# Kernel optimization log

Measured on AMD Instinct MI355X. Metric: run time of the kernel, lower is better.

## Reference

```python
import jax, jax.numpy as jnp
import numpy as np

NEG_BIG = -1e9

def setup_inputs() -> dict:
    key = jax.random.key(0)
    kq, kk, kv, kwq, kwk, kwv, km = jax.random.split(key, 7)
    B, S, d = 16, 1024, 512
    Q = jax.random.normal(kq, (B, S, d), dtype=jnp.float32)
    K = jax.random.normal(kk, (B, S, d), dtype=jnp.float32)
    V = jax.random.normal(kv, (B, S, d), dtype=jnp.float32)
    # nn.Linear weights [d, d]; torch applies x @ W.T
    WQ = jax.random.normal(kwq, (d, d), dtype=jnp.float32) / np.sqrt(d)
    WK = jax.random.normal(kwk, (d, d), dtype=jnp.float32) / np.sqrt(d)
    WV = jax.random.normal(kwv, (d, d), dtype=jnp.float32) / np.sqrt(d)
    mask = jax.random.randint(km, (B, S), 0, 2, dtype=jnp.int32)
    return {"Q": Q, "K": K, "V": V, "WQ": WQ, "WK": WK, "WV": WV, "mask": mask}


def reference(Q, K, V, WQ, WK, WV, mask):
    d = Q.shape[-1]
    q = jnp.einsum('bsd,ed->bse', Q, WQ)
    k = jnp.einsum('bsd,ed->bse', K, WK)
    v = jnp.einsum('bsd,ed->bse', V, WV)
    scores = jnp.einsum('bqd,bkd->bqk', q, k) / jnp.sqrt(jnp.float32(d))
    attn = jax.nn.softmax(scores, axis=-1)
    # Faithful to original: mask applied AFTER softmax with -1e9 fill
    m = mask[:, None, :]  # [B,1,S] broadcast over query dim
    attn = jnp.where(m == 0, jnp.float32(NEG_BIG), attn)
    out = jnp.einsum('bqk,bkd->bqd', attn, v)
    return (out, attn)
```

## Files before the change

kernel.cpp:

```cpp
#include <hip/hip_runtime.h>
#include <hip/hip_bf16.h>

typedef float f32x4 __attribute__((ext_vector_type(4)));
typedef __bf16 bf16x8 __attribute__((ext_vector_type(8)));
typedef unsigned short u16x8 __attribute__((ext_vector_type(8)));
typedef int i32x4 __attribute__((ext_vector_type(4)));

#define NEG_BIG_F (-1000000000.0f)
#define SCALE_F 0.044194173824159216f

__device__ __forceinline__ unsigned short f2bf(float f) {
  unsigned int u = __float_as_uint(f);
  u += 0x7FFFu + ((u >> 16) & 1u);
  return (unsigned short)(u >> 16);
}

__device__ __forceinline__ float bf2f(unsigned short h) {
  return __uint_as_float((unsigned int)h << 16);
}

__device__ __forceinline__ u16x8 cvt8(f32x4 a, f32x4 b) {
  u16x8 r;
  r[0] = f2bf(a[0]); r[1] = f2bf(a[1]); r[2] = f2bf(a[2]); r[3] = f2bf(a[3]);
  r[4] = f2bf(b[0]); r[5] = f2bf(b[1]); r[6] = f2bf(b[2]); r[7] = f2bf(b[3]);
  return r;
}

__device__ __forceinline__ void gload16(const void* g, char* l) {
  __builtin_amdgcn_global_load_lds(
      (const __attribute__((address_space(1))) unsigned int*)g,
      (__attribute__((address_space(3))) unsigned int*)l, 16, 0, 0);
}

__global__ __launch_bounds__(256) void cvtW(
    const float* __restrict__ w0, const float* __restrict__ w1,
    const float* __restrict__ w2, unsigned short* __restrict__ out)
{
  const float* src = blockIdx.z == 0 ? w0 : (blockIdx.z == 1 ? w1 : w2);
  unsigned short* dst = out + (size_t)blockIdx.z * 262144;
  const int i = (blockIdx.x * 256 + threadIdx.x) * 8;
  f32x4 a = *(const f32x4*)(src + i);
  f32x4 b = *(const f32x4*)(src + i + 4);
  *(u16x8*)&dst[i] = cvt8(a, b);
}

__global__ __launch_bounds__(512, 2) void proj_all(
    const float* __restrict__ Q, const float* __restrict__ Kx,
    const float* __restrict__ V, const unsigned short* __restrict__ wb,
    unsigned short* __restrict__ qb, unsigned short* __restrict__ kb,
    unsigned short* __restrict__ vt)
{
  __shared__ __align__(16) unsigned short lds[32768];

  const int bid = blockIdx.x;
  const int tid = threadIdx.x;
  const int lane = tid & 63, wave = tid >> 6;
  const int fr = lane & 15, fq = lane >> 4;

  if (bid < 256) {
    const int z = bid >> 7, rem = bid & 127;
    const float* X = z ? Kx : Q;
    const unsigned short* W = wb + (size_t)z * 262144;
    unsigned short* Y = z ? kb : qb;
    const int m0 = (rem & 63) * 256, n0 = (rem >> 6) * 256;
    const int wr = (wave >> 2) * 128, wc = (wave & 3) * 64;

    unsigned short (*As)[256][32] = (unsigned short (*)[256][32])lds;
    unsigned short (*Bs)[256][32] = (unsigned short (*)[256][32])(lds + 16384);

    f32x4 acc[8][4] = {};

    int arow_s[2], aswz_s[2];
    const float* gAs[2];
    #pragma unroll
    for (int i = 0; i < 2; i++) {
      const int c = tid + 512 * i;
      arow_s[i] = c >> 2;
      aswz_s[i] = ((c & 3) ^ ((arow_s[i] >> 1) & 3)) * 8;
      gAs[i] = X + (size_t)(m0 + arow_s[i]) * 512 + (c & 3) * 8;
    }
    const unsigned short* gB[2]; char* lB[2];
    #pragma unroll
    for (int i = 0; i < 2; i++) {
      const int c = tid + 512 * i, row = c >> 2, slot = c & 3;
      gB[i] = W + (size_t)(n0 + row) * 512 + (slot ^ ((row >> 1) & 3)) * 8;
      lB[i] = (char*)(lds + 16384) + c * 16;
    }

    f32x4 pa[2][2][2];
    #pragma unroll
    for (int i = 0; i < 2; i++) {
      pa[0][i][0] = *(const f32x4*)(gAs[i]);
      pa[0][i][1] = *(const f32x4*)(gAs[i] + 4);
      pa[1][i][0] = *(const f32x4*)(gAs[i] + 32);
      pa[1][i][1] = *(const f32x4*)(gAs[i] + 36);
    }
    #pragma unroll
    for (int i = 0; i < 2; i++) gload16(gB[i], lB[i]);
    #pragma unroll
    for (int i = 0; i < 2; i++)
      *(u16x8*)&As[0][arow_s[i]][aswz_s[i]] = cvt8(pa[0][i][0], pa[0][i][1]);

    #pragma unroll
    for (int t = 0; t < 16; t++) {
      const int cur = t & 1, nxt = cur ^ 1;
      const int kt = t * 32;
      if (t < 15) {
        #pragma unroll
        for (int i = 0; i < 2; i++) gload16(gB[i] + kt + 32, lB[i] + nxt * 16384);
      }
      if (t < 14) {
        #pragma unroll
        for (int i = 0; i < 2; i++) {
          pa[cur][i][0] = *(const f32x4*)(gAs[i] + kt + 64);
          pa[cur][i][1] = *(const f32x4*)(gAs[i] + kt + 68);
        }
      }
      if (t == 0 || t == 14)
        asm volatile("s_waitcnt vmcnt(6) lgkmcnt(0)" ::: "memory");
      else if (t == 15)
        asm volatile("s_waitcnt vmcnt(0) lgkmcnt(0)" ::: "memory");
      else
        asm volatile("s_waitcnt vmcnt(10) lgkmcnt(0)" ::: "memory");
      __builtin_amdgcn_sched_barrier(0);
      __builtin_amdgcn_s_barrier();

      bf16x8 bv[4];
      #pragma unroll
      for (int nf = 0; nf < 4; nf++) {
        const int br = wc + nf * 16 + fr;
        bv[nf] = *(const bf16x8*)&Bs[cur][br][(fq ^ ((br >> 1) & 3)) * 8];
      }
      #pragma unroll
      for (int mf = 0; mf < 8; mf++) {
        const int ar = wr + mf * 16 + fr;
        bf16x8 av = *(const bf16x8*)&As[cur][ar][(fq ^ ((ar >> 1) & 3)) * 8];
        #pragma unroll
        for (int nf = 0; nf < 4; nf++)
          acc[mf][nf] = __builtin_amdgcn_mfma_f32_16x16x32_bf16(av, bv[nf], acc[mf][nf], 0, 0, 0);
      }

      if (t < 15) {
        #pragma unroll
        for (int i = 0; i < 2; i++)
          *(u16x8*)&As[nxt][arow_s[i]][aswz_s[i]] = cvt8(pa[nxt][i][0], pa[nxt][i][1]);
      }
      __builtin_amdgcn_s_barrier();
    }

    #pragma unroll
    for (int mf = 0; mf < 8; mf++)
      #pragma unroll
      for (int nf = 0; nf < 4; nf++)
        #pragma unroll
        for (int rr = 0; rr < 4; rr++) {
          const int m = m0 + wr + mf * 16 + fq * 4 + rr;
          const int n = n0 + wc + nf * 16 + fr;
          Y[(size_t)m * 512 + n] = f2bf(acc[mf][nf][rr]);
        }
  } else {
    const int c0 = bid - 256;
    const int m0 = (c0 & 3) * 128, n0 = ((c0 >> 2) & 3) * 256, b = c0 >> 4;
    const int wr = (wave >> 2) * 64, wc = (wave & 3) * 64;
    const unsigned short* wv = wb + 524288;

    unsigned short (*As)[128][32] = (unsigned short (*)[128][32])lds;
    unsigned short (*Bs)[256][32] = (unsigned short (*)[256][32])(lds + 8192);

    f32x4 acc[4][4] = {};

    const int ar_s = tid >> 2, aslot = tid & 3;
    const unsigned short* gA = wv + (size_t)(m0 + ar_s) * 512 + (aslot ^ ((ar_s >> 1) & 3)) * 8;
    char* lA = (char*)lds + tid * 16;

    int brow_s[2], bswz_s[2];
    const float* gBs[2];
    #pragma unroll
    for (int i = 0; i < 2; i++) {
      const int c = tid + 512 * i;
      brow_s[i] = c >> 2;
      bswz_s[i] = ((c & 3) ^ ((brow_s[i] >> 1) & 3)) * 8;
      gBs[i] = V + ((size_t)b * 1024 + n0 + brow_s[i]) * 512 + (c & 3) * 8;
    }

    f32x4 pb[2][2][2];
    #pragma unroll
    for (int i = 0; i < 2; i++) {
      pb[0][i][0] = *(const f32x4*)(gBs[i]);
      pb[0][i][1] = *(const f32x4*)(gBs[i] + 4);
      pb[1][i][0] = *(const f32x4*)(gBs[i] + 32);
      pb[1][i][1] = *(const f32x4*)(gBs[i] + 36);
    }
    gload16(gA, lA);
    #pragma unroll
    for (int i = 0; i < 2; i++)
      *(u16x8*)&Bs[0][brow_s[i]][bswz_s[i]] = cvt8(pb[0][i][0], pb[0][i][1]);

    #pragma unroll
    for (int t = 0; t < 16; t++) {
      const int cur = t & 1, nxt = cur ^ 1;
      const int kt = t * 32;
      if (t < 15) gload16(gA + kt + 32, lA + nxt * 8192);
      if (t < 14) {
        #pragma unroll
        for (int i = 0; i < 2; i++) {
          pb[cur][i][0] = *(const f32x4*)(gBs[i] + kt + 64);
          pb[cur][i][1] = *(const f32x4*)(gBs[i] + kt + 68);
        }
      }
      if (t == 0 || t == 14)
        asm volatile("s_waitcnt vmcnt(5) lgkmcnt(0)" ::: "memory");
      else if (t == 15)
        asm volatile("s_waitcnt vmcnt(0) lgkmcnt(0)" ::: "memory");
      else
        asm volatile("s_waitcnt vmcnt(9) lgkmcnt(0)" ::: "memory");
      __builtin_amdgcn_sched_barrier(0);
      __builtin_amdgcn_s_barrier();

      bf16x8 av[4], bv[4];
      #pragma unroll
      for (int mf = 0; mf < 4; mf++) {
        const int ar = wr + mf * 16 + fr;
        av[mf] = *(const bf16x8*)&As[cur][ar][(fq ^ ((ar >> 1) & 3)) * 8];
      }
      #pragma unroll
      for (int nf = 0; nf < 4; nf++) {
        const int br = wc + nf * 16 + fr;
        bv[nf] = *(const bf16x8*)&Bs[cur][br][(fq ^ ((br >> 1) & 3)) * 8];
      }
      #pragma unroll
      for (int mf = 0; mf < 4; mf++)
        #pragma unroll
        for (int nf = 0; nf < 4; nf++)
          acc[mf][nf] = __builtin_amdgcn_mfma_f32_16x16x32_bf16(av[mf], bv[nf], acc[mf][nf], 0, 0, 0);

      if (t < 15) {
        #pragma unroll
        for (int i = 0; i < 2; i++)
          *(u16x8*)&Bs[nxt][brow_s[i]][bswz_s[i]] = cvt8(pb[nxt][i][0], pb[nxt][i][1]);
      }
      __builtin_amdgcn_s_barrier();
    }

    #pragma unroll
    for (int mf = 0; mf < 4; mf++)
      #pragma unroll
      for (int nf = 0; nf < 4; nf++)
        #pragma unroll
        for (int rr = 0; rr < 4; rr++) {
          const int e = m0 + wr + mf * 16 + fq * 4 + rr;
          const int s = n0 + wc + nf * 16 + fr;
          vt[((size_t)b * 512 + e) * 1024 + s] = f2bf(acc[mf][nf][rr]);
        }
  }
}

__global__ __launch_bounds__(512, 2) void score256(
    const unsigned short* __restrict__ qb, const unsigned short* __restrict__ kb,
    const int* __restrict__ mask,
    unsigned short* __restrict__ P, float* __restrict__ partial)
{
  __shared__ __align__(16) unsigned short As[2][256][32];
  __shared__ __align__(16) unsigned short Bs[2][256][32];

  const int tid = threadIdx.x, bz = blockIdx.z;
  const int m0 = blockIdx.x * 256, n0 = blockIdx.y * 256;
  const int lane = tid & 63, wave = tid >> 6;
  const int wr = (wave >> 2) * 128, wc = (wave & 3) * 64;
  const int fr = lane & 15, fq = lane >> 4;

  f32x4 acc[8][4] = {};

  const unsigned short* gA[2]; char* lA[2];
  const unsigned short* gB[2]; char* lB[2];
  #pragma unroll
  for (int i = 0; i < 2; i++) {
    const int c = tid + 512 * i, row = c >> 2, slot = c & 3;
    const int sw = (slot ^ ((row >> 1) & 3)) * 8;
    gA[i] = qb + ((size_t)bz * 1024 + m0 + row) * 512 + sw;
    gB[i] = kb + ((size_t)bz * 1024 + n0 + row) * 512 + sw;
    lA[i] = (char*)&As[0][0][0] + c * 16;
    lB[i] = (char*)&Bs[0][0][0] + c * 16;
  }

  #pragma unroll
  for (int i = 0; i < 2; i++) { gload16(gA[i], lA[i]); gload16(gB[i], lB[i]); }

  int cur = 0;
  for (int kt = 0; kt < 512; kt += 32) {
    const int nb = cur ^ 1;
    if (kt < 480) {
      #pragma unroll
      for (int i = 0; i < 2; i++) {
        gload16(gA[i] + kt + 32, lA[i] + nb * 16384);
        gload16(gB[i] + kt + 32, lB[i] + nb * 16384);
      }
      asm volatile("s_waitcnt vmcnt(4) lgkmcnt(0)" ::: "memory");
    } else {
      asm volatile("s_waitcnt vmcnt(0) lgkmcnt(0)" ::: "memory");
    }
    __builtin_amdgcn_sched_barrier(0);
    __builtin_amdgcn_s_barrier();

    bf16x8 bv[4];
    #pragma unroll
    for (int nf = 0; nf < 4; nf++) {
      const int br = wc + nf * 16 + fr;
      bv[nf] = *(const bf16x8*)&Bs[cur][br][(fq ^ ((br >> 1) & 3)) * 8];
    }
    #pragma unroll
    for (int mf = 0; mf < 8; mf++) {
      const int ar = wr + mf * 16 + fr;
      bf16x8 av = *(const bf16x8*)&As[cur][ar][(fq ^ ((ar >> 1) & 3)) * 8];
      #pragma unroll
      for (int nf = 0; nf < 4; nf++)
        acc[mf][nf] = __builtin_amdgcn_mfma_f32_16x16x32_bf16(av, bv[nf], acc[mf][nf], 0, 0, 0);
    }
    __builtin_amdgcn_s_barrier();
    cur = nb;
  }

  int mcol[4];
  #pragma unroll
  for (int nf = 0; nf < 4; nf++)
    mcol[nf] = mask[bz * 1024 + n0 + wc + nf * 16 + fr];

  unsigned short* Pb = P + ((size_t)bz << 20);
  const int slot = blockIdx.y * 4 + (wave & 3);
  #pragma unroll
  for (int mf = 0; mf < 8; mf++) {
    #pragma unroll
    for (int rr = 0; rr < 4; rr++) {
      const int m = m0 + wr + mf * 16 + fq * 4 + rr;
      float e = 0.f;
      #pragma unroll
      for (int nf = 0; nf < 4; nf++) {
        const float ev = __expf(acc[mf][nf][rr] * SCALE_F);
        e += ev;
        Pb[(size_t)m * 1024 + n0 + wc + nf * 16 + fr] =
            mcol[nf] ? f2bf(ev) : (unsigned short)0;
      }
      e += __shfl_xor(e, 1); e += __shfl_xor(e, 2);
      e += __shfl_xor(e, 4); e += __shfl_xor(e, 8);
      if (fr == 0)
        partial[(size_t)slot * 16384 + bz * 1024 + m] = e;
    }
  }
}

__global__ __launch_bounds__(256) void mv_attn(
    const unsigned short* __restrict__ vt, const unsigned short* __restrict__ P,
    const float* __restrict__ partial, const int* __restrict__ mask,
    float* __restrict__ mvsum, float* __restrict__ attn)
{
  const int bid = blockIdx.x;
  const int tid = threadIdx.x;
  if (bid < 2048) {
    const int row = bid * 4 + (tid >> 6);
    const int b = row >> 9;
    const int lane = tid & 63;
    const unsigned short* vr = vt + (size_t)row * 1024 + lane * 16;
    const int* mr = mask + b * 1024 + lane * 16;
    u16x8 v0 = *(const u16x8*)(vr);
    u16x8 v1 = *(const u16x8*)(vr + 8);
    float s = 0.f;
    #pragma unroll
    for (int j = 0; j < 8; j++) {
      if (!mr[j])     s += bf2f(v0[j]);
      if (!mr[8 + j]) s += bf2f(v1[j]);
    }
    #pragma unroll
    for (int o = 32; o > 0; o >>= 1) s += __shfl_xor(s, o);
    if (lane == 0) mvsum[row] = s;
  } else {
    const int ab = bid - 2048;
    __shared__ float s_inv[2];
    const int row0 = ab * 2;
    if (tid < 2) {
      float s = 0.f;
      #pragma unroll
      for (int p = 0; p < 16; p++) s += partial[(size_t)p * 16384 + row0 + tid];
      s_inv[tid] = 1.0f / s;
    }
    __syncthreads();
    const size_t base = (size_t)ab * 2048 + tid * 8;
    const int b = (int)(base >> 20);
    const int k0 = (int)(base & 1023);
    const u16x8 p8 = *(const u16x8*)(P + base);
    const float iv = s_inv[tid >> 7];
    const int* mr = mask + b * 1024 + k0;
    const i32x4 ma = *(const i32x4*)(mr);
    const i32x4 mb = *(const i32x4*)(mr + 4);
    f32x4 o0, o1;
    o0[0] = ma[0] ? bf2f(p8[0]) * iv : NEG_BIG_F;
    o0[1] = ma[1] ? bf2f(p8[1]) * iv : NEG_BIG_F;
    o0[2] = ma[2] ? bf2f(p8[2]) * iv : NEG_BIG_F;
    o0[3] = ma[3] ? bf2f(p8[3]) * iv : NEG_BIG_F;
    o1[0] = mb[0] ? bf2f(p8[4]) * iv : NEG_BIG_F;
    o1[1] = mb[1] ? bf2f(p8[5]) * iv : NEG_BIG_F;
    o1[2] = mb[2] ? bf2f(p8[6]) * iv : NEG_BIG_F;
    o1[3] = mb[3] ? bf2f(p8[7]) * iv : NEG_BIG_F;
    *(f32x4*)(attn + base) = o0;
    *(f32x4*)(attn + base + 4) = o1;
  }
}

__global__ __launch_bounds__(512) void pv_gemm(
    const unsigned short* __restrict__ P, const unsigned short* __restrict__ vt,
    const float* __restrict__ partial, const float* __restrict__ mvsum,
    float* __restrict__ out)
{
  __shared__ __align__(16) unsigned short As[2][64][32];
  __shared__ __align__(16) unsigned short Bs[2][512][32];
  __shared__ float inv_l[64];

  const int tid = threadIdx.x;
  const int bz = blockIdx.z, m0 = blockIdx.x * 64;
  const int lane = tid & 63, wave = tid >> 6;
  const int n0 = wave * 64;
  const int fr = lane & 15, fq = lane >> 4;

  f32x4 acc[4][4] = {};

  if (tid < 64) {
    float s = 0.f;
    #pragma unroll
    for (int p = 0; p < 16; p++) s += partial[(size_t)p * 16384 + bz * 1024 + m0 + tid];
    inv_l[tid] = 1.0f / s;
  }

  const unsigned short* gA = nullptr; char* lA = nullptr;
  if (tid < 256) {
    const int row = tid >> 2, slot = tid & 3;
    gA = P + ((size_t)bz << 20) + (size_t)(m0 + row) * 1024 + (slot ^ ((row >> 1) & 3)) * 8;
    lA = (char*)&As[0][0][0] + tid * 16;
  }
  const unsigned short* gB[4]; char* lB[4];
  #pragma unroll
  for (int i = 0; i < 4; i++) {
    const int c = tid + 512 * i, row = c >> 2, slot = c & 3;
    gB[i] = vt + ((size_t)bz * 512 + row) * 1024 + (slot ^ ((row >> 1) & 3)) * 8;
    lB[i] = (char*)&Bs[0][0][0] + c * 16;
  }

  if (tid < 256) gload16(gA, lA);
  #pragma unroll
  for (int i = 0; i < 4; i++) gload16(gB[i], lB[i]);

  int cur = 0;
  for (int t = 0; t < 32; t++) {
    const int nb = cur ^ 1;
    const int kt = t * 32;
    if (t < 31) {
      if (tid < 256) gload16(gA + kt + 32, lA + nb * 4096);
      #pragma unroll
      for (int i = 0; i < 4; i++) gload16(gB[i] + kt + 32, lB[i] + nb * 32768);
      if (wave < 4) asm volatile("s_waitcnt vmcnt(5) lgkmcnt(0)" ::: "memory");
      else          asm volatile("s_waitcnt vmcnt(4) lgkmcnt(0)" ::: "memory");
    } else {
      asm volatile("s_waitcnt vmcnt(0) lgkmcnt(0)" ::: "memory");
    }
    __builtin_amdgcn_sched_barrier(0);
    __builtin_amdgcn_s_barrier();

    bf16x8 af[4], bv[4];
    #pragma unroll
    for (int mf = 0; mf < 4; mf++) {
      const int ar = mf * 16 + fr;
      af[mf] = *(const bf16x8*)&As[cur][ar][(fq ^ ((ar >> 1) & 3)) * 8];
    }
    #pragma unroll
    for (int nf = 0; nf < 4; nf++) {
      const int br = n0 + nf * 16 + fr;
      bv[nf] = *(const bf16x8*)&Bs[cur][br][(fq ^ ((br >> 1) & 3)) * 8];
    }
    #pragma unroll
    for (int mf = 0; mf < 4; mf++)
      #pragma unroll
      for (int nf = 0; nf < 4; nf++)
        acc[mf][nf] = __builtin_amdgcn_mfma_f32_16x16x32_bf16(af[mf], bv[nf], acc[mf][nf], 0, 0, 0);
    __builtin_amdgcn_s_barrier();
    cur = nb;
  }

  float mvv[4];
  #pragma unroll
  for (int nf = 0; nf < 4; nf++)
    mvv[nf] = mvsum[bz * 512 + n0 + nf * 16 + fr];
  #pragma unroll
  for (int mf = 0; mf < 4; mf++)
    #pragma unroll
    for (int rr = 0; rr < 4; rr++) {
      const int m = m0 + mf * 16 + fq * 4 + rr;
      const float iv = inv_l[mf * 16 + fq * 4 + rr];
      #pragma unroll
      for (int nf = 0; nf < 4; nf++)
        out[((size_t)bz * 1024 + m) * 512 + n0 + nf * 16 + fr] =
            iv * acc[mf][nf][rr] + NEG_BIG_F * mvv[nf];
    }
}

extern "C" void kernel_launch(void* const* d_in, const int* in_sizes, int n_in,
                              void* d_out, int out_size, void* d_ws, size_t ws_size,
                              hipStream_t stream)
{
  const float* Q  = (const float*)d_in[0];
  const float* Kx = (const float*)d_in[1];
  const float* V  = (const float*)d_in[2];
  const float* WQ = (const float*)d_in[3];
  const float* WK = (const float*)d_in[4];
  const float* WV = (const float*)d_in[5];
  const int* mask = (const int*)d_in[6];

  const int B = 16, S = 1024, D = 512;
  float* out_f  = (float*)d_out;
  float* attn_f = out_f + (size_t)B * S * D;
  unsigned short* Pbuf = (unsigned short*)d_out;

  unsigned short* qb = (unsigned short*)d_ws;
  unsigned short* kb = qb + (size_t)B * S * D;
  unsigned short* vt = kb + (size_t)B * S * D;
  unsigned short* wb = vt + (size_t)B * S * D;
  float* partial = (float*)(wb + 786432);
  float* mvsum = partial + 262144;

  cvtW<<<dim3(128, 1, 3), 256, 0, stream>>>(WQ, WK, WV, wb);
  proj_all<<<dim3(512), 512, 0, stream>>>(Q, Kx, V, wb, qb, kb, vt);
  score256<<<dim3(4, 4, 16), 512, 0, stream>>>(qb, kb, mask, Pbuf, partial);
  mv_attn<<<dim3(10240), 256, 0, stream>>>(vt, Pbuf, partial, mask, mvsum, attn_f);
  pv_gemm<<<dim3(16, 1, 16), 512, 0, stream>>>(Pbuf, vt, partial, mvsum, out_f);
}
```

Baseline: 147.0 us.

## Fuse attn output into PV GEMM and masked-V sum into score kernel

The separate mv_attn kernel is removed. The masked column sums of V now run as extra blocks of the score kernel, which moves to a 1D grid with manually decoded tile indices. The normalized, masked attention matrix is now written from inside the PV GEMM loop, using the P tile already staged in shared memory. This drops one kernel launch and a second full read of P from global memory. In exchange, the GEMM main loop carries extra global stores and mask loads, and an extra __syncthreads is added before the loop.

```diff
diff --git a/kernel.cpp b/kernel.cpp
--- a/kernel.cpp
+++ b/kernel.cpp
@@ -4,6 +4,7 @@
 typedef float f32x4 __attribute__((ext_vector_type(4)));
 typedef __bf16 bf16x8 __attribute__((ext_vector_type(8)));
 typedef unsigned short u16x8 __attribute__((ext_vector_type(8)));
+typedef unsigned short u16x4 __attribute__((ext_vector_type(4)));
 typedef int i32x4 __attribute__((ext_vector_type(4)));
 
 #define NEG_BIG_F (-1000000000.0f)
@@ -255,16 +256,40 @@
   }
 }
 
-__global__ __launch_bounds__(512, 2) void score256(
+__global__ __launch_bounds__(512, 2) void score_mv(
     const unsigned short* __restrict__ qb, const unsigned short* __restrict__ kb,
-    const int* __restrict__ mask,
-    unsigned short* __restrict__ P, float* __restrict__ partial)
+    const unsigned short* __restrict__ vt, const int* __restrict__ mask,
+    unsigned short* __restrict__ P, float* __restrict__ partial,
+    float* __restrict__ mvsum)
 {
   __shared__ __align__(16) unsigned short As[2][256][32];
   __shared__ __align__(16) unsigned short Bs[2][256][32];
 
-  const int tid = threadIdx.x, bz = blockIdx.z;
-  const int m0 = blockIdx.x * 256, n0 = blockIdx.y * 256;
+  const int bid = blockIdx.x;
+  const int tid = threadIdx.x;
+
+  if (bid >= 256) {
+    const int row = (bid - 256) * 8 + (tid >> 6);
+    const int b = row >> 9;
+    const int lane = tid & 63;
+    const unsigned short* vr = vt + (size_t)row * 1024 + lane * 16;
+    const int* mr = mask + b * 1024 + lane * 16;
+    u16x8 v0 = *(const u16x8*)(vr);
+    u16x8 v1 = *(const u16x8*)(vr + 8);
+    float s = 0.f;
+    #pragma unroll
+    for (int j = 0; j < 8; j++) {
+      if (!mr[j])     s += bf2f(v0[j]);
+      if (!mr[8 + j]) s += bf2f(v1[j]);
+    }
+    #pragma unroll
+    for (int o = 32; o > 0; o >>= 1) s += __shfl_xor(s, o);
+    if (lane == 0) mvsum[row] = s;
+    return;
+  }
+
+  const int bz = bid >> 4;
+  const int m0 = (bid & 3) * 256, n0 = ((bid >> 2) & 3) * 256;
   const int lane = tid & 63, wave = tid >> 6;
   const int wr = (wave >> 2) * 128, wc = (wave & 3) * 64;
   const int fr = lane & 15, fq = lane >> 4;
@@ -326,7 +351,7 @@
     mcol[nf] = mask[bz * 1024 + n0 + wc + nf * 16 + fr];
 
   unsigned short* Pb = P + ((size_t)bz << 20);
-  const int slot = blockIdx.y * 4 + (wave & 3);
+  const int slot = ((bid >> 2) & 3) * 4 + (wave & 3);
   #pragma unroll
   for (int mf = 0; mf < 8; mf++) {
     #pragma unroll
@@ -348,67 +373,11 @@
   }
 }
 
-__global__ __launch_bounds__(256) void mv_attn(
-    const unsigned short* __restrict__ vt, const unsigned short* __restrict__ P,
-    const float* __restrict__ partial, const int* __restrict__ mask,
-    float* __restrict__ mvsum, float* __restrict__ attn)
-{
-  const int bid = blockIdx.x;
-  const int tid = threadIdx.x;
-  if (bid < 2048) {
-    const int row = bid * 4 + (tid >> 6);
-    const int b = row >> 9;
-    const int lane = tid & 63;
-    const unsigned short* vr = vt + (size_t)row * 1024 + lane * 16;
-    const int* mr = mask + b * 1024 + lane * 16;
-    u16x8 v0 = *(const u16x8*)(vr);
-    u16x8 v1 = *(const u16x8*)(vr + 8);
-    float s = 0.f;
-    #pragma unroll
-    for (int j = 0; j < 8; j++) {
-      if (!mr[j])     s += bf2f(v0[j]);
-      if (!mr[8 + j]) s += bf2f(v1[j]);
-    }
-    #pragma unroll
-    for (int o = 32; o > 0; o >>= 1) s += __shfl_xor(s, o);
-    if (lane == 0) mvsum[row] = s;
-  } else {
-    const int ab = bid - 2048;
-    __shared__ float s_inv[2];
-    const int row0 = ab * 2;
-    if (tid < 2) {
-      float s = 0.f;
-      #pragma unroll
-      for (int p = 0; p < 16; p++) s += partial[(size_t)p * 16384 + row0 + tid];
-      s_inv[tid] = 1.0f / s;
-    }
-    __syncthreads();
-    const size_t base = (size_t)ab * 2048 + tid * 8;
-    const int b = (int)(base >> 20);
-    const int k0 = (int)(base & 1023);
-    const u16x8 p8 = *(const u16x8*)(P + base);
-    const float iv = s_inv[tid >> 7];
-    const int* mr = mask + b * 1024 + k0;
-    const i32x4 ma = *(const i32x4*)(mr);
-    const i32x4 mb = *(const i32x4*)(mr + 4);
-    f32x4 o0, o1;
-    o0[0] = ma[0] ? bf2f(p8[0]) * iv : NEG_BIG_F;
-    o0[1] = ma[1] ? bf2f(p8[1]) * iv : NEG_BIG_F;
-    o0[2] = ma[2] ? bf2f(p8[2]) * iv : NEG_BIG_F;
-    o0[3] = ma[3] ? bf2f(p8[3]) * iv : NEG_BIG_F;
-    o1[0] = mb[0] ? bf2f(p8[4]) * iv : NEG_BIG_F;
-    o1[1] = mb[1] ? bf2f(p8[5]) * iv : NEG_BIG_F;
-    o1[2] = mb[2] ? bf2f(p8[6]) * iv : NEG_BIG_F;
-    o1[3] = mb[3] ? bf2f(p8[7]) * iv : NEG_BIG_F;
-    *(f32x4*)(attn + base) = o0;
-    *(f32x4*)(attn + base + 4) = o1;
-  }
-}
-
-__global__ __launch_bounds__(512) void pv_gemm(
+__global__ __launch_bounds__(512) void pv_attn(
     const unsigned short* __restrict__ P, const unsigned short* __restrict__ vt,
     const float* __restrict__ partial, const float* __restrict__ mvsum,
-    float* __restrict__ out)
+    const int* __restrict__ mask,
+    float* __restrict__ out, float* __restrict__ attn)
 {
   __shared__ __align__(16) unsigned short As[2][64][32];
   __shared__ __align__(16) unsigned short Bs[2][512][32];
@@ -443,9 +412,15 @@
     lB[i] = (char*)&Bs[0][0][0] + c * 16;
   }
 
+  const int arow = tid >> 3, acol = (tid & 7) * 4;
+  const int aslot8 = ((acol >> 3) ^ ((arow >> 1) & 3)) * 8 + (acol & 7);
+  float* arp = attn + ((size_t)bz * 1024 + m0 + arow) * 1024 + acol;
+  const int* mrp = mask + bz * 1024 + acol;
+
   if (tid < 256) gload16(gA, lA);
   #pragma unroll
   for (int i = 0; i < 4; i++) gload16(gB[i], lB[i]);
+  __syncthreads();
 
   int cur = 0;
   for (int t = 0; t < 32; t++) {
@@ -479,6 +454,18 @@
       #pragma unroll
       for (int nf = 0; nf < 4; nf++)
         acc[mf][nf] = __builtin_amdgcn_mfma_f32_16x16x32_bf16(af[mf], bv[nf], acc[mf][nf], 0, 0, 0);
+
+    {
+      const u16x4 pv4 = *(const u16x4*)&As[cur][arow][aslot8];
+      const i32x4 mv = *(const i32x4*)(mrp + kt);
+      const float iv = inv_l[arow];
+      f32x4 o;
+      o[0] = mv[0] ? bf2f(pv4[0]) * iv : NEG_BIG_F;
+      o[1] = mv[1] ? bf2f(pv4[1]) * iv : NEG_BIG_F;
+      o[2] = mv[2] ? bf2f(pv4[2]) * iv : NEG_BIG_F;
+      o[3] = mv[3] ? bf2f(pv4[3]) * iv : NEG_BIG_F;
+      *(f32x4*)(arp + kt) = o;
+    }
     __builtin_amdgcn_s_barrier();
     cur = nb;
   }
@@ -526,7 +513,6 @@
 
   cvtW<<<dim3(128, 1, 3), 256, 0, stream>>>(WQ, WK, WV, wb);
   proj_all<<<dim3(512), 512, 0, stream>>>(Q, Kx, V, wb, qb, kb, vt);
-  score256<<<dim3(4, 4, 16), 512, 0, stream>>>(qb, kb, mask, Pbuf, partial);
-  mv_attn<<<dim3(10240), 256, 0, stream>>>(vt, Pbuf, partial, mask, mvsum, attn_f);
-  pv_gemm<<<dim3(16, 1, 16), 512, 0, stream>>>(Pbuf, vt, partial, mvsum, out_f);
-}
+  score_mv<<<dim3(1280), 512, 0, stream>>>(qb, kb, vt, mask, Pbuf, partial, mvsum);
+  pv_attn<<<dim3(16, 1, 16), 512, 0, stream>>>(Pbuf, vt, partial, mvsum, mask, out_f, attn_f);
+}
```

After: 143.3 us. 2.5% less time.
